# Performance work log

Measured on AMD Instinct MI355X. Metric: run time of the kernel, lower is better.

Reference implementation:

```python
import jax, jax.numpy as jnp
import numpy as np

NUM_HOPS = 4
N_NODES = 50000
N_EDGES = 500000
D = 128
H1 = 256
INIT_A, INIT_B = -0.01, 0.01


def _mlp(x, w1, b1, w2, b2):
    # Linear -> ReLU -> Linear -> ReLU (Dropout is identity in eval mode)
    h = jax.nn.relu(x @ w1 + b1)
    return jax.nn.relu(h @ w2 + b2)


def _uniform(key, shape):
    return jax.random.uniform(key, shape, jnp.float32, INIT_A, INIT_B)


def setup_inputs() -> dict:
    key = jax.random.key(0)
    ks = jax.random.split(key, 40)
    inp = {
        "batch_token": jax.random.normal(ks[0], (N_NODES, D), jnp.float32),
        "edge_p_node": jax.random.randint(ks[1], (N_EDGES,), 0, N_NODES),
        "edge_c_node": jax.random.randint(ks[2], (N_EDGES,), 0, N_NODES),
        "edge_p_indicate": jax.random.uniform(ks[3], (N_EDGES,), jnp.float32),
        "edge_c_indicate": jax.random.uniform(ks[4], (N_EDGES,), jnp.float32),
        "p_mask": jax.random.uniform(ks[5], (N_NODES,), jnp.float32),
        "c_mask": jax.random.uniform(ks[6], (N_NODES,), jnp.float32),
        "start_token": jax.random.normal(ks[7], (D,), jnp.float32),
        "end_token": jax.random.normal(ks[8], (D,), jnp.float32),
    }
    # MLP_V: D -> H1 -> D ; MLP_E: 1 -> H1 -> D ; MLP_p/c/aggr: 3D -> H1 -> D
    k = 9
    for name, din in (("V", D), ("E", 1), ("P", 3 * D), ("C", 3 * D), ("A", 3 * D)):
        inp[name + "w1"] = _uniform(ks[k], (din, H1)); k += 1
        inp[name + "b1"] = _uniform(ks[k], (H1,)); k += 1
        inp[name + "w2"] = _uniform(ks[k], (H1, D)); k += 1
        inp[name + "b2"] = _uniform(ks[k], (D,)); k += 1
    return inp


def reference(batch_token, edge_p_node, edge_c_node, edge_p_indicate,
              edge_c_indicate, p_mask, c_mask, start_token, end_token,
              Vw1, Vb1, Vw2, Vb2, Ew1, Eb1, Ew2, Eb2,
              Pw1, Pb1, Pw2, Pb2, Cw1, Cb1, Cw2, Cb2,
              Aw1, Ab1, Aw2, Ab2):
    n = batch_token.shape[0]
    h = _mlp(batch_token, Vw1, Vb1, Vw2, Vb2)  # [N, D]
    edge_p = _mlp(edge_p_indicate[:, None], Ew1, Eb1, Ew2, Eb2)  # [E, D]
    edge_c = _mlp(edge_c_indicate[:, None], Ew1, Eb1, Ew2, Eb2)  # [E, D]
    ones_e = jnp.ones((edge_p_node.shape[0],), jnp.float32)
    cnt_p = jnp.clip(jax.ops.segment_sum(ones_e, edge_p_node, num_segments=n), 1.0)
    cnt_c = jnp.clip(jax.ops.segment_sum(ones_e, edge_c_node, num_segments=n), 1.0)
    for _ in range(NUM_HOPS - 1):
        hp = h[edge_p_node]  # [E, D]
        hc = h[edge_c_node]  # [E, D]
        s_p = _mlp(jnp.concatenate([hc, hp, edge_p], -1), Pw1, Pb1, Pw2, Pb2)
        s_c = _mlp(jnp.concatenate([hp, hc, edge_c], -1), Cw1, Cb1, Cw2, Cb2)
        s_p = jax.ops.segment_sum(s_p, edge_p_node, num_segments=n) / cnt_p[:, None]
        s_c = jax.ops.segment_sum(s_c, edge_c_node, num_segments=n) / cnt_c[:, None]
        s_p = s_p + p_mask[:, None] * start_token
        s_c = s_c + c_mask[:, None] * end_token
        x_aggr = jnp.concatenate([h, s_p, s_c], -1)  # [N, 3D]
        h = jax.nn.relu(h + _mlp(x_aggr, Aw1, Ab1, Aw2, Ab2))
    return h
```

## Files before the change

### kernel.cpp

```cpp
#include <hip/hip_runtime.h>
#include <hip/hip_bf16.h>
#include <cstdint>
#include <cstddef>
#include <cmath>

typedef __bf16 bf16;
typedef bf16 bf16x8 __attribute__((ext_vector_type(8)));
typedef float f32x4 __attribute__((ext_vector_type(4)));

#define D_DIM 128
#define NB 32
#define EB 64
#define TS 136
#define XS 264
#define SRS 132
#define AS 392

__device__ __forceinline__ f32x4 mfma16(bf16x8 a, bf16x8 b, f32x4 c) {
  return __builtin_amdgcn_mfma_f32_16x16x32_bf16(a, b, c, 0, 0, 0);
}

__device__ __forceinline__ int clampi(int v, int hi) {
  return v < 0 ? 0 : (v > hi ? hi : v);
}

__device__ __forceinline__ void stage16(const float* __restrict__ src, bf16* dst) {
  bf16 tmp[16];
#pragma unroll
  for (int q = 0; q < 4; ++q) {
    f32x4 f = ((const f32x4*)src)[q];
#pragma unroll
    for (int j = 0; j < 4; ++j) tmp[q * 4 + j] = (bf16)f[j];
  }
  *(bf16x8*)dst = *(bf16x8*)tmp;
  *(bf16x8*)(dst + 8) = *(bf16x8*)(tmp + 8);
}

template <int NSEG>
__device__ __forceinline__ void mlp_layer1(const bf16* s0, const bf16* s1, const bf16* s2,
                                           const int S,
                                           const bf16* __restrict__ W1t,
                                           const float* __restrict__ B1,
                                           bf16* x2, const int lane, const int w) {
  const int col = lane & 15, quad = lane >> 4;
  const int K = NSEG * 128;
  f32x4 acc[2][4] = {};
  const bf16* segs[3] = {s0, s1, s2};
#pragma unroll
  for (int sg = 0; sg < NSEG; ++sg) {
    const bf16* xl = segs[sg];
#pragma unroll
    for (int kk = 0; kk < 128; kk += 32) {
      const int k0 = sg * 128 + kk;
      bf16x8 a0 = *(const bf16x8*)&xl[col * S + kk + quad * 8];
      bf16x8 a1 = *(const bf16x8*)&xl[(col + 16) * S + kk + quad * 8];
#pragma unroll
      for (int nt = 0; nt < 4; ++nt) {
        bf16x8 b = *(const bf16x8*)(W1t + (size_t)(w * 64 + nt * 16 + col) * K + k0 + quad * 8);
        acc[0][nt] = mfma16(a0, b, acc[0][nt]);
        acc[1][nt] = mfma16(a1, b, acc[1][nt]);
      }
    }
  }
#pragma unroll
  for (int nt = 0; nt < 4; ++nt) {
    const int n = w * 64 + nt * 16 + col;
    const float b1 = B1[n];
#pragma unroll
    for (int mt = 0; mt < 2; ++mt)
#pragma unroll
      for (int i = 0; i < 4; ++i) {
        float v = acc[mt][nt][i] + b1;
        x2[(mt * 16 + quad * 4 + i) * XS + n] = (bf16)(v > 0.f ? v : 0.f);
      }
  }
}

__device__ __forceinline__ void mlp_layer2(const bf16* x2, const bf16* __restrict__ W2t,
                                           const int lane, const int w, f32x4 acc2[2][2]) {
  const int col = lane & 15, quad = lane >> 4;
#pragma unroll
  for (int k0 = 0; k0 < 256; k0 += 32) {
    bf16x8 a0 = *(const bf16x8*)&x2[col * XS + k0 + quad * 8];
    bf16x8 a1 = *(const bf16x8*)&x2[(col + 16) * XS + k0 + quad * 8];
#pragma unroll
    for (int nt = 0; nt < 2; ++nt) {
      bf16x8 b = *(const bf16x8*)(W2t + (size_t)(w * 32 + nt * 16 + col) * 256 + k0 + quad * 8);
      acc2[0][nt] = mfma16(a0, b, acc2[0][nt]);
      acc2[1][nt] = mfma16(a1, b, acc2[1][nt]);
    }
  }
}

__device__ __forceinline__ void emit_z(const bf16* x, const int S,
                                       const bf16* __restrict__ Pw1t,
                                       const bf16* __restrict__ Cw1t,
                                       bf16* __restrict__ Zbuf,
                                       const int r0, const int N,
                                       const int lane, const int w) {
  const int col = lane & 15, quad = lane >> 4;
  const bf16* base = ((w & 2) ? Cw1t : Pw1t) + (w & 1) * 128;
  bf16* out = Zbuf + (size_t)w * ((size_t)N * 256);
#pragma unroll
  for (int half = 0; half < 2; ++half) {
    f32x4 acc[2][8] = {};
#pragma unroll
    for (int kc = 0; kc < 4; ++kc) {
      bf16x8 a0 = *(const bf16x8*)&x[col * S + kc * 32 + quad * 8];
      bf16x8 a1 = *(const bf16x8*)&x[(col + 16) * S + kc * 32 + quad * 8];
#pragma unroll
      for (int nt = 0; nt < 8; ++nt) {
        const int n = half * 128 + nt * 16 + col;
        bf16x8 b = *(const bf16x8*)(base + (size_t)n * 384 + kc * 32 + quad * 8);
        acc[0][nt] = mfma16(a0, b, acc[0][nt]);
        acc[1][nt] = mfma16(a1, b, acc[1][nt]);
      }
    }
#pragma unroll
    for (int nt = 0; nt < 8; ++nt) {
      const int n = half * 128 + nt * 16 + col;
#pragma unroll
      for (int mt = 0; mt < 2; ++mt)
#pragma unroll
        for (int i = 0; i < 4; ++i) {
          int g = r0 + mt * 16 + quad * 4 + i;
          if (g < N) out[(size_t)g * 256 + n] = (bf16)acc[mt][nt][i];
        }
    }
  }
}


__global__ void transpose_kernel(const float* __restrict__ in, bf16* __restrict__ out,
                                 int K, int N) {
  int k = blockIdx.x * blockDim.x + threadIdx.x;
  int n = blockIdx.y;
  if (k < K) out[(size_t)n * K + k] = (bf16)in[(size_t)k * N + n];
}

__global__ void count_kernel(const int* __restrict__ epn, const int* __restrict__ ecn,
                             int* cntp, int* cntc, int E, int N) {
  int i = blockIdx.x * blockDim.x + threadIdx.x;
  if (i < E) {
    atomicAdd(&cntp[clampi(epn[i], N - 1)], 1);
    atomicAdd(&cntc[clampi(ecn[i], N - 1)], 1);
  }
}

__global__ void inv_kernel(const int* __restrict__ cntp, const int* __restrict__ cntc,
                           float* invp, float* invc, int N) {
  int i = blockIdx.x * blockDim.x + threadIdx.x;
  if (i < N) {
    invp[i] = 1.f / fmaxf((float)cntp[i], 1.f);
    invc[i] = 1.f / fmaxf((float)cntc[i], 1.f);
  }
}

__global__ void scan_pair_kernel(const int* __restrict__ cntp, const int* __restrict__ cntc,
                                 int* __restrict__ offp, int* __restrict__ offc, int n) {
  const int* cnt = blockIdx.x ? cntc : cntp;
  int* offs = blockIdx.x ? offc : offp;
  __shared__ int buf[1024];
  __shared__ int carry;
  const int t = threadIdx.x;
  if (t == 0) carry = 0;
  __syncthreads();
  for (int base = 0; base < n; base += 1024) {
    int v = (base + t < n) ? cnt[base + t] : 0;
    buf[t] = v;
    __syncthreads();
    for (int d = 1; d < 1024; d <<= 1) {
      int add = (t >= d) ? buf[t - d] : 0;
      __syncthreads();
      buf[t] += add;
      __syncthreads();
    }
    if (base + t < n) offs[base + t] = carry + buf[t] - v;
    __syncthreads();
    if (t == 1023) carry += buf[1023];
    __syncthreads();
  }
}

__global__ void scatter_kernel(const int* __restrict__ epn, const int* __restrict__ ecn,
                               const int* __restrict__ offp, const int* __restrict__ offc,
                               int* curp, int* curc, int* sortp, int* sortc, int E, int N) {
  int i = blockIdx.x * blockDim.x + threadIdx.x;
  if (i < E) {
    int p = clampi(epn[i], N - 1);
    sortp[offp[p] + atomicAdd(&curp[p], 1)] = i;
    int c = clampi(ecn[i], N - 1);
    sortc[offc[c] + atomicAdd(&curc[c], 1)] = i;
  }
}


__global__ __launch_bounds__(256) void emlp_table_kernel(
    const float* __restrict__ Ew1, const float* __restrict__ Eb1,
    const float* __restrict__ Ew2, const float* __restrict__ Eb2,
    float* __restrict__ ts_out, float* __restrict__ Atab, float* __restrict__ Btab) {
  __shared__ float s_tk[256], s_w[256], s_b[256];
  __shared__ int s_k[256];
  __shared__ float sA[256], sB[256];
  const int j = blockIdx.x;
  const int t = threadIdx.x;
  float w = Ew1[t], b = Eb1[t];
  float tk = (w != 0.f) ? (-b / w) : INFINITY;
  s_tk[t] = tk; s_w[t] = w; s_b[t] = b;
  __syncthreads();
  int rank = 0;
  for (int u = 0; u < 256; ++u) {
    float tu = s_tk[u];
    if (tu < tk || (tu == tk && u < t)) ++rank;
  }
  s_k[rank] = t;
  if (j == 0) ts_out[rank] = tk;
  float w2own = Ew2[(size_t)t * 128 + j];
  bool act = (w < 0.f || (w == 0.f && b > 0.f));
  sA[t] = act ? w * w2own : 0.f;
  sB[t] = act ? b * w2own : 0.f;
  __syncthreads();
  for (int d = 128; d > 0; d >>= 1) {
    if (t < d) { sA[t] += sA[t + d]; sB[t] += sB[t + d]; }
    __syncthreads();
  }
  const float baseA = sA[0], baseB = sB[0];
  __syncthreads();
  int k = s_k[t];
  float wk = s_w[k], bk = s_b[k];
  float dA = 0.f, dB = 0.f;
  if (wk != 0.f) {
    float w2 = Ew2[(size_t)k * 128 + j];
    float sgn = wk > 0.f ? 1.f : -1.f;
    dA = sgn * wk * w2;
    dB = sgn * bk * w2;
  }
  sA[t] = dA; sB[t] = dB;
  __syncthreads();
  for (int d = 1; d < 256; d <<= 1) {
    float aA = (t >= d) ? sA[t - d] : 0.f;
    float aB = (t >= d) ? sB[t - d] : 0.f;
    __syncthreads();
    sA[t] += aA; sB[t] += aB;
    __syncthreads();
  }
  const float eb2 = Eb2[j];
  if (t == 0) { Atab[j] = baseA; Btab[j] = baseB + eb2; }
  Atab[(size_t)(t + 1) * 128 + j] = baseA + sA[t];
  Btab[(size_t)(t + 1) * 128 + j] = baseB + sB[t] + eb2;
}


__global__ __launch_bounds__(256, 2) void node_v_kernel(
    const float* __restrict__ bt, const bf16* __restrict__ W1t, const float* __restrict__ B1,
    const bf16* __restrict__ W2t, const float* __restrict__ B2,
    const bf16* __restrict__ Pw1t, const bf16* __restrict__ Cw1t,
    bf16* __restrict__ Zbuf, float* __restrict__ hout, int N) {
  __shared__ __attribute__((aligned(16))) bf16 x[NB * TS];
  __shared__ __attribute__((aligned(16))) bf16 x2[NB * XS];
  const int t = threadIdx.x;
  const int r0 = blockIdx.x * NB;
  {
    const int r = t >> 3, c0 = (t & 7) * 16;
    int g = r0 + r; if (g >= N) g = N - 1;
    stage16(bt + (size_t)g * D_DIM + c0, &x[r * TS + c0]);
  }
  __syncthreads();
  const int lane = t & 63, w = t >> 6, col = lane & 15, quad = lane >> 4;
  mlp_layer1<1>(x, x, x, TS, W1t, B1, x2, lane, w);
  __syncthreads();
  f32x4 acc2[2][2] = {};
  mlp_layer2(x2, W2t, lane, w, acc2);
  __syncthreads();
#pragma unroll
  for (int nt = 0; nt < 2; ++nt) {
    const int n = w * 32 + nt * 16 + col;
    const float b2 = B2[n];
#pragma unroll
    for (int mt = 0; mt < 2; ++mt)
#pragma unroll
      for (int i = 0; i < 4; ++i) {
        int m = mt * 16 + quad * 4 + i;
        int g = r0 + m;
        float v = acc2[mt][nt][i] + b2;
        v = v > 0.f ? v : 0.f;
        x[m * TS + n] = (bf16)v;
        if (g < N) hout[(size_t)g * D_DIM + n] = v;
      }
  }
  __syncthreads();
  emit_z(x, TS, Pw1t, Cw1t, Zbuf, r0, N, lane, w);
}


__global__ __launch_bounds__(256, 3) void edge_side_kernel(
    const bf16* __restrict__ Zbuf,
    const float* __restrict__ epi, const float* __restrict__ eci,
    const int* __restrict__ epn, const int* __restrict__ ecn,
    const int* __restrict__ sortp, const int* __restrict__ sortc,
    const float* __restrict__ ets, const float* __restrict__ Atab,
    const float* __restrict__ Btab,
    const bf16* __restrict__ Pw1t, const float* __restrict__ Pb1,
    const bf16* __restrict__ Pw2t, const float* __restrict__ Pb2,
    const bf16* __restrict__ Cw1t, const float* __restrict__ Cb1,
    const bf16* __restrict__ Cw2t, const float* __restrict__ Cb2,
    float* __restrict__ accp, float* __restrict__ accc, int E, int N) {
  const int side = blockIdx.y;
  const size_t NZ = (size_t)N * 256;
  const bf16* ZO     = Zbuf + (size_t)(side * 2 + 0) * NZ;
  const bf16* ZW     = Zbuf + (size_t)(side * 2 + 1) * NZ;
  const float* ei    = side ? eci : epi;
  const int* own_n   = side ? ecn : epn;
  const int* oth_n   = side ? epn : ecn;
  const int* sorted  = side ? sortc : sortp;
  const bf16* W1c    = (side ? Cw1t : Pw1t) + 256;
  const float* B1    = side ? Cb1 : Pb1;
  const bf16* W2t    = side ? Cw2t : Pw2t;
  const float* B2    = side ? Cb2 : Pb2;
  float* acc         = side ? accc : accp;

  __shared__ int s_own[EB], s_oth[EB];
  __shared__ float s_x[EB];
  __shared__ float s_ts[256];
  __shared__ __attribute__((aligned(16))) bf16 feat[EB * TS];
  __shared__ __attribute__((aligned(16))) char xbuf[EB * XS * 2];
  bf16* xz = (bf16*)xbuf;
  float* sred = (float*)xbuf;

  const int t = threadIdx.x;
  const int e0 = blockIdx.x * EB;
  s_ts[t] = ets[t];
  if (t < EB) {
    int e = e0 + t;
    if (e < E) {
      int id = clampi(sorted[e], E - 1);
      s_own[t] = clampi(own_n[id], N - 1);
      s_oth[t] = clampi(oth_n[id], N - 1);
      s_x[t] = ei[id];
    } else {
      s_own[t] = -1; s_oth[t] = 0; s_x[t] = 0.f;
    }
  }
  __syncthreads();

  const int lane = t & 63, w = t >> 6, col = lane & 15, quad = lane >> 4;

  bf16x8 va[8];
  const int zr = t >> 2, zc = (t & 3) * 64;
  const bf16* pw_s;
  {
    int ro = s_oth[zr];
    const bf16* po = ZO + (size_t)ro * 256 + zc;
#pragma unroll
    for (int q = 0; q < 8; ++q) va[q] = *(const bf16x8*)(po + q * 8);
    int rw = s_own[zr]; if (rw < 0) rw = 0;
    pw_s = ZW + (size_t)rw * 256 + zc;
  }

  {
    const int r = zr, c0 = (t & 3) * 32;
    const float xv = s_x[r];
    int lo = 0, hi = 256;
#pragma unroll
    for (int it = 0; it < 8; ++it) {
      int mid = (lo + hi) >> 1;
      if (s_ts[mid] < xv) lo = mid + 1; else hi = mid;
    }
    const float* Ar = Atab + (size_t)lo * 128 + c0;
    const float* Br = Btab + (size_t)lo * 128 + c0;
#pragma unroll
    for (int q = 0; q < 4; ++q) {
      f32x4 a0 = *(const f32x4*)(Ar + q * 8);
      f32x4 a1 = *(const f32x4*)(Ar + q * 8 + 4);
      f32x4 b0 = *(const f32x4*)(Br + q * 8);
      f32x4 b1v = *(const f32x4*)(Br + q * 8 + 4);
      bf16 o[8];
#pragma unroll
      for (int j = 0; j < 4; ++j) {
        float v0 = fmaf(xv, a0[j], b0[j]);
        float v1 = fmaf(xv, a1[j], b1v[j]);
        o[j] = (bf16)(v0 > 0.f ? v0 : 0.f);
        o[4 + j] = (bf16)(v1 > 0.f ? v1 : 0.f);
      }
      *(bf16x8*)&feat[r * TS + c0 + q * 8] = *(bf16x8*)o;
    }
  }

  {
#pragma unroll
    for (int q = 0; q < 8; ++q) {
      bf16x8 b = *(const bf16x8*)(pw_s + q * 8);
      bf16 o[8];
#pragma unroll
      for (int j = 0; j < 8; ++j) o[j] = (bf16)((float)va[q][j] + (float)b[j]);
      *(bf16x8*)&xz[zr * XS + zc + q * 8] = *(bf16x8*)o;
    }
  }
  __syncthreads();

  {
    f32x4 acc1[4][4] = {};
#pragma unroll
    for (int kc = 0; kc < 4; ++kc) {
      bf16x8 afr[4];
#pragma unroll
      for (int g = 0; g < 4; ++g)
        afr[g] = *(const bf16x8*)&feat[(g * 16 + col) * TS + kc * 32 + quad * 8];
#pragma unroll
      for (int nt = 0; nt < 4; ++nt) {
        const int n = w * 64 + nt * 16 + col;
        bf16x8 b = *(const bf16x8*)(W1c + (size_t)n * 384 + kc * 32 + quad * 8);
#pragma unroll
        for (int g = 0; g < 4; ++g) acc1[g][nt] = mfma16(afr[g], b, acc1[g][nt]);
      }
    }
#pragma unroll
    for (int nt = 0; nt < 4; ++nt) {
      const int n = w * 64 + nt * 16 + col;
      const float b1 = B1[n];
#pragma unroll
      for (int g = 0; g < 4; ++g)
#pragma unroll
        for (int i = 0; i < 4; ++i) {
          const int m = g * 16 + quad * 4 + i;
          float v = acc1[g][nt][i] + b1 + (float)xz[m * XS + n];
          xz[m * XS + n] = (bf16)(v > 0.f ? v : 0.f);
        }
    }
  }
  __syncthreads();

  f32x4 acc2[4][2] = {};
#pragma unroll
  for (int kc = 0; kc < 8; ++kc) {
    bf16x8 afr[4];
#pragma unroll
    for (int g = 0; g < 4; ++g)
      afr[g] = *(const bf16x8*)&xz[(g * 16 + col) * XS + kc * 32 + quad * 8];
#pragma unroll
    for (int nt = 0; nt < 2; ++nt) {
      const int n = w * 32 + nt * 16 + col;
      bf16x8 b = *(const bf16x8*)(W2t + (size_t)n * 256 + kc * 32 + quad * 8);
#pragma unroll
      for (int g = 0; g < 4; ++g) acc2[g][nt] = mfma16(afr[g], b, acc2[g][nt]);
    }
  }
  __syncthreads();

#pragma unroll
  for (int nt = 0; nt < 2; ++nt) {
    const int n = w * 32 + nt * 16 + col;
    const float b2 = B2[n];
#pragma unroll
    for (int g = 0; g < 4; ++g)
#pragma unroll
      for (int i = 0; i < 4; ++i) {
        float v = acc2[g][nt][i] + b2;
        sred[(g * 16 + quad * 4 + i) * SRS + n] = v > 0.f ? v : 0.f;
      }
  }
  {
    const int c = w * 32 + (lane >> 1);
    const int rlo = (lane & 1) * 32;
    float run = 0.f;
    int cur = s_own[rlo];
    for (int r = rlo; r < rlo + 32; ++r) {
      int k = s_own[r];
      if (k != cur) {
        if (cur >= 0)
          __hip_atomic_fetch_add(&acc[(size_t)cur * D_DIM + c], run,
                                 __ATOMIC_RELAXED, __HIP_MEMORY_SCOPE_AGENT);
        run = 0.f;
        cur = k;
      }
      run += sred[r * SRS + c];
    }
    if (cur >= 0)
      __hip_atomic_fetch_add(&acc[(size_t)cur * D_DIM + c], run,
                             __ATOMIC_RELAXED, __HIP_MEMORY_SCOPE_AGENT);
  }
}


__global__ __launch_bounds__(256, 2) void node_a_kernel(
    const float* __restrict__ h, const float* __restrict__ accp, const float* __restrict__ accc,
    const float* __restrict__ invp, const float* __restrict__ invc,
    const float* __restrict__ pmask, const float* __restrict__ cmask,
    const float* __restrict__ stok, const float* __restrict__ etok,
    const bf16* __restrict__ W1t, const float* __restrict__ B1,
    const bf16* __restrict__ W2t, const float* __restrict__ B2,
    const bf16* __restrict__ Pw1t, const bf16* __restrict__ Cw1t,
    bf16* __restrict__ Zbuf, int emitZ,
    float* __restrict__ hout, int N) {
  __shared__ __attribute__((aligned(16))) bf16 x[NB * AS];
  __shared__ __attribute__((aligned(16))) bf16 x2[NB * XS];
  const int t = threadIdx.x;
  const int r0 = blockIdx.x * NB;
  {
    const int r = t >> 3, c0 = (t & 7) * 16;
    int g = r0 + r; if (g >= N) g = N - 1;
    stage16(h + (size_t)g * D_DIM + c0, &x[r * AS + c0]);
  }
  {
    const int j = t;
    for (int r = 0; r < NB; ++r) {
      int g = r0 + r; if (g >= N) g = N - 1;
      float v;
      if (j < 128)
        v = accp[(size_t)g * D_DIM + j] * invp[g] + pmask[g] * stok[j];
      else {
        int jj = j - 128;
        v = accc[(size_t)g * D_DIM + jj] * invc[g] + cmask[g] * etok[jj];
      }
      x[r * AS + 128 + j] = (bf16)v;
    }
  }
  __syncthreads();
  const int lane = t & 63, w = t >> 6, col = lane & 15, quad = lane >> 4;
  mlp_layer1<3>(x, x + 128, x + 256, AS, W1t, B1, x2, lane, w);
  __syncthreads();
  f32x4 acc2[2][2] = {};
  mlp_layer2(x2, W2t, lane, w, acc2);
  __syncthreads();
#pragma unroll
  for (int nt = 0; nt < 2; ++nt) {
    const int n = w * 32 + nt * 16 + col;
    const float b2 = B2[n];
#pragma unroll
    for (int mt = 0; mt < 2; ++mt)
#pragma unroll
      for (int i = 0; i < 4; ++i) {
        int m = mt * 16 + quad * 4 + i;
        int g = r0 + m;
        int gc = g < N ? g : N - 1;
        float mlpv = acc2[mt][nt][i] + b2;
        mlpv = mlpv > 0.f ? mlpv : 0.f;
        float v = h[(size_t)gc * D_DIM + n] + mlpv;
        v = v > 0.f ? v : 0.f;
        x[m * AS + n] = (bf16)v;
        if (g < N) hout[(size_t)g * D_DIM + n] = v;
      }
  }
  if (emitZ) {
    __syncthreads();
    emit_z(x, AS, Pw1t, Cw1t, Zbuf, r0, N, lane, w);
  }
}


extern "C" void kernel_launch(void* const* d_in, const int* in_sizes, int n_in,
                              void* d_out, int out_size, void* d_ws, size_t ws_size,
                              hipStream_t stream) {
  const float* batch_token = (const float*)d_in[0];
  const int* epn = (const int*)d_in[1];
  const int* ecn = (const int*)d_in[2];
  const float* epi = (const float*)d_in[3];
  const float* eci = (const float*)d_in[4];
  const float* pmask = (const float*)d_in[5];
  const float* cmask = (const float*)d_in[6];
  const float* stok = (const float*)d_in[7];
  const float* etok = (const float*)d_in[8];
  const float *Vw1 = (const float*)d_in[9], *Vb1 = (const float*)d_in[10],
              *Vw2 = (const float*)d_in[11], *Vb2 = (const float*)d_in[12];
  const float *Ew1 = (const float*)d_in[13], *Eb1 = (const float*)d_in[14],
              *Ew2 = (const float*)d_in[15], *Eb2 = (const float*)d_in[16];
  const float *Pw1 = (const float*)d_in[17], *Pb1 = (const float*)d_in[18],
              *Pw2 = (const float*)d_in[19], *Pb2 = (const float*)d_in[20];
  const float *Cw1 = (const float*)d_in[21], *Cb1 = (const float*)d_in[22],
              *Cw2 = (const float*)d_in[23], *Cb2 = (const float*)d_in[24];
  const float *Aw1 = (const float*)d_in[25], *Ab1 = (const float*)d_in[26],
              *Aw2 = (const float*)d_in[27], *Ab2 = (const float*)d_in[28];
  const int N = in_sizes[5];
  const int E = in_sizes[1];

  char* ws = (char*)d_ws;
  size_t off = 0;
  auto alloc = [&](size_t bytes) {
    size_t o = off;
    off += (bytes + 511) & ~(size_t)511;
    return o;
  };
  float* accp = (float*)(ws + alloc((size_t)N * D_DIM * 4));
  float* accc = (float*)(ws + alloc((size_t)N * D_DIM * 4));
  bf16* Zbuf = (bf16*)(ws + alloc((size_t)4 * N * 256 * 2));
  float* invp = (float*)(ws + alloc((size_t)N * 4));
  float* invc = (float*)(ws + alloc((size_t)N * 4));
  int* cntp = (int*)(ws + alloc((size_t)N * 4));
  int* cntc = (int*)(ws + alloc((size_t)N * 4));
  int* offp = (int*)(ws + alloc((size_t)N * 4));
  int* offc = (int*)(ws + alloc((size_t)N * 4));
  int* curp = (int*)(ws + alloc((size_t)N * 4));
  int* curc = (int*)(ws + alloc((size_t)N * 4));
  int* sortp = (int*)(ws + alloc((size_t)E * 4));
  int* sortc = (int*)(ws + alloc((size_t)E * 4));
  bf16* Vw1t = (bf16*)(ws + alloc(128 * 256 * 2));
  bf16* Pw1t = (bf16*)(ws + alloc(384 * 256 * 2));
  bf16* Cw1t = (bf16*)(ws + alloc(384 * 256 * 2));
  bf16* Aw1t = (bf16*)(ws + alloc(384 * 256 * 2));
  bf16* Vw2t = (bf16*)(ws + alloc(256 * 128 * 2));
  bf16* Pw2t = (bf16*)(ws + alloc(256 * 128 * 2));
  bf16* Cw2t = (bf16*)(ws + alloc(256 * 128 * 2));
  bf16* Aw2t = (bf16*)(ws + alloc(256 * 128 * 2));
  float* ets  = (float*)(ws + alloc(256 * 4));
  float* Atab = (float*)(ws + alloc((size_t)257 * 128 * 4));
  float* Btab = (float*)(ws + alloc((size_t)257 * 128 * 4));
  float* hbuf = (float*)d_out;
  (void)ws_size; (void)n_in; (void)out_size;

  const dim3 blk(256);
  transpose_kernel<<<dim3(1, 256), blk, 0, stream>>>(Vw1, Vw1t, 128, 256);
  transpose_kernel<<<dim3(2, 256), blk, 0, stream>>>(Pw1, Pw1t, 384, 256);
  transpose_kernel<<<dim3(2, 256), blk, 0, stream>>>(Cw1, Cw1t, 384, 256);
  transpose_kernel<<<dim3(2, 256), blk, 0, stream>>>(Aw1, Aw1t, 384, 256);
  transpose_kernel<<<dim3(1, 128), blk, 0, stream>>>(Vw2, Vw2t, 256, 128);
  transpose_kernel<<<dim3(1, 128), blk, 0, stream>>>(Pw2, Pw2t, 256, 128);
  transpose_kernel<<<dim3(1, 128), blk, 0, stream>>>(Cw2, Cw2t, 256, 128);
  transpose_kernel<<<dim3(1, 128), blk, 0, stream>>>(Aw2, Aw2t, 256, 128);

  emlp_table_kernel<<<dim3(128), dim3(256), 0, stream>>>(Ew1, Eb1, Ew2, Eb2, ets, Atab, Btab);

  const size_t cntbytes = (size_t)((char*)(cntc + N) - (char*)cntp);
  hipMemsetAsync(cntp, 0, cntbytes, stream);
  count_kernel<<<dim3((E + 255) / 256), blk, 0, stream>>>(epn, ecn, cntp, cntc, E, N);
  inv_kernel<<<dim3((N + 255) / 256), blk, 0, stream>>>(cntp, cntc, invp, invc, N);
  scan_pair_kernel<<<dim3(2), dim3(1024), 0, stream>>>(cntp, cntc, offp, offc, N);
  const size_t curbytes = (size_t)((char*)(curc + N) - (char*)curp);
  hipMemsetAsync(curp, 0, curbytes, stream);
  scatter_kernel<<<dim3((E + 255) / 256), blk, 0, stream>>>(epn, ecn, offp, offc,
                                                            curp, curc, sortp, sortc, E, N);

  const int nblocks = (N + NB - 1) / NB;
  const int eblocks = (E + EB - 1) / EB;

  node_v_kernel<<<dim3(nblocks), blk, 0, stream>>>(
      batch_token, Vw1t, Vb1, Vw2t, Vb2, Pw1t, Cw1t, Zbuf, hbuf, N);

  const size_t accbytes = (size_t)((char*)(accc + (size_t)N * D_DIM) - (char*)accp);
  for (int hop = 0; hop < 3; ++hop) {
    hipMemsetAsync(accp, 0, accbytes, stream);
    edge_side_kernel<<<dim3(eblocks, 2), blk, 0, stream>>>(
        Zbuf, epi, eci, epn, ecn, sortp, sortc, ets, Atab, Btab,
        Pw1t, Pb1, Pw2t, Pb2, Cw1t, Cb1, Cw2t, Cb2, accp, accc, E, N);
    node_a_kernel<<<dim3(nblocks), blk, 0, stream>>>(
        hbuf, accp, accc, invp, invc, pmask, cmask, stok, etok,
        Aw1t, Ab1, Aw2t, Ab2, Pw1t, Cw1t, Zbuf, (hop < 2) ? 1 : 0, hbuf, N);
  }
}
```

Measured before the change: 2.398 ms.

## Compute edge features directly into MFMA fragments and raise occupancy bounds

The edge kernel no longer builds the edge-feature tile in shared memory. Each lane now computes its own A-fragments for the first GEMM straight from the Atab/Btab lookup tables, which removes the 17 KB feat buffer and its LDS round trip. Launch bounds go up (edge 3→4 waves/SIMD, node kernels 2→3) to exploit the freed LDS and raise occupancy. The cost is that each wave recomputes the features and rereads the table rows from global memory, 4 times per fragment, and the tighter register budget could cause spills.

```diff
diff --git a/kernel.cpp b/kernel.cpp
--- a/kernel.cpp
+++ b/kernel.cpp
@@ -251,7 +251,7 @@
 }
 
 
-__global__ __launch_bounds__(256, 2) void node_v_kernel(
+__global__ __launch_bounds__(256, 3) void node_v_kernel(
     const float* __restrict__ bt, const bf16* __restrict__ W1t, const float* __restrict__ B1,
     const bf16* __restrict__ W2t, const float* __restrict__ B2,
     const bf16* __restrict__ Pw1t, const bf16* __restrict__ Cw1t,
@@ -293,7 +293,7 @@
 }
 
 
-__global__ __launch_bounds__(256, 3) void edge_side_kernel(
+__global__ __launch_bounds__(256, 4) void edge_side_kernel(
     const bf16* __restrict__ Zbuf,
     const float* __restrict__ epi, const float* __restrict__ eci,
     const int* __restrict__ epn, const int* __restrict__ ecn,
@@ -322,7 +322,6 @@
   __shared__ int s_own[EB], s_oth[EB];
   __shared__ float s_x[EB];
   __shared__ float s_ts[256];
-  __shared__ __attribute__((aligned(16))) bf16 feat[EB * TS];
   __shared__ __attribute__((aligned(16))) char xbuf[EB * XS * 2];
   bf16* xz = (bf16*)xbuf;
   float* sred = (float*)xbuf;
@@ -357,33 +356,19 @@
     pw_s = ZW + (size_t)rw * 256 + zc;
   }
 
-  {
-    const int r = zr, c0 = (t & 3) * 32;
-    const float xv = s_x[r];
+  int lo4[4];
+  float xv4[4];
+#pragma unroll
+  for (int g = 0; g < 4; ++g) {
+    const float xv = s_x[g * 16 + col];
     int lo = 0, hi = 256;
 #pragma unroll
     for (int it = 0; it < 8; ++it) {
       int mid = (lo + hi) >> 1;
       if (s_ts[mid] < xv) lo = mid + 1; else hi = mid;
     }
-    const float* Ar = Atab + (size_t)lo * 128 + c0;
-    const float* Br = Btab + (size_t)lo * 128 + c0;
-#pragma unroll
-    for (int q = 0; q < 4; ++q) {
-      f32x4 a0 = *(const f32x4*)(Ar + q * 8);
-      f32x4 a1 = *(const f32x4*)(Ar + q * 8 + 4);
-      f32x4 b0 = *(const f32x4*)(Br + q * 8);
-      f32x4 b1v = *(const f32x4*)(Br + q * 8 + 4);
-      bf16 o[8];
-#pragma unroll
-      for (int j = 0; j < 4; ++j) {
-        float v0 = fmaf(xv, a0[j], b0[j]);
-        float v1 = fmaf(xv, a1[j], b1v[j]);
-        o[j] = (bf16)(v0 > 0.f ? v0 : 0.f);
-        o[4 + j] = (bf16)(v1 > 0.f ? v1 : 0.f);
-      }
-      *(bf16x8*)&feat[r * TS + c0 + q * 8] = *(bf16x8*)o;
-    }
+    lo4[g] = lo;
+    xv4[g] = xv;
   }
 
   {
@@ -404,8 +389,23 @@
     for (int kc = 0; kc < 4; ++kc) {
       bf16x8 afr[4];
 #pragma unroll
-      for (int g = 0; g < 4; ++g)
-        afr[g] = *(const bf16x8*)&feat[(g * 16 + col) * TS + kc * 32 + quad * 8];
+      for (int g = 0; g < 4; ++g) {
+        const float* Ar = Atab + (size_t)lo4[g] * 128 + kc * 32 + quad * 8;
+        const float* Br = Btab + (size_t)lo4[g] * 128 + kc * 32 + quad * 8;
+        f32x4 a0 = *(const f32x4*)Ar;
+        f32x4 a1 = *(const f32x4*)(Ar + 4);
+        f32x4 b0 = *(const f32x4*)Br;
+        f32x4 b1v = *(const f32x4*)(Br + 4);
+        bf16 av[8];
+#pragma unroll
+        for (int j = 0; j < 4; ++j) {
+          float v0 = fmaf(xv4[g], a0[j], b0[j]);
+          float v1 = fmaf(xv4[g], a1[j], b1v[j]);
+          av[j] = (bf16)(v0 > 0.f ? v0 : 0.f);
+          av[4 + j] = (bf16)(v1 > 0.f ? v1 : 0.f);
+        }
+        afr[g] = *(bf16x8*)av;
+      }
 #pragma unroll
       for (int nt = 0; nt < 4; ++nt) {
         const int n = w * 64 + nt * 16 + col;
@@ -482,7 +482,7 @@
 }
 
 
-__global__ __launch_bounds__(256, 2) void node_a_kernel(
+__global__ __launch_bounds__(256, 3) void node_a_kernel(
     const float* __restrict__ h, const float* __restrict__ accp, const float* __restrict__ accc,
     const float* __restrict__ invp, const float* __restrict__ invc,
     const float* __restrict__ pmask, const float* __restrict__ cmask,
```

After: 3.438 ms. 43.4% more time.
